# Optimization experiments

Hardware: AMD Instinct MI355X
Metric: run time of the kernel (lower is better)

The kernel has to match this reference:

```python
import jax, jax.numpy as jnp
import numpy as np

D_IN = 1024
D_OUT = 1024
NUM_HEADS = 16
HEAD_DIM = D_OUT // NUM_HEADS


def setup_inputs() -> dict:
    key = jax.random.key(0)
    ks = jax.random.split(key, 6)
    s = 0.02
    x = jax.random.normal(ks[0], (1, 4096, D_IN), dtype=jnp.float32)
    W_q = jax.random.normal(ks[1], (D_IN, D_OUT), dtype=jnp.float32) * s
    W_k = jax.random.normal(ks[2], (D_IN, D_OUT), dtype=jnp.float32) * s
    W_v = jax.random.normal(ks[3], (D_IN, D_OUT), dtype=jnp.float32) * s
    W_o = jax.random.normal(ks[4], (D_OUT, D_OUT), dtype=jnp.float32) * s
    b_o = jnp.zeros((D_OUT,), dtype=jnp.float32)
    return {"x": x, "W_q": W_q, "W_k": W_k, "W_v": W_v, "W_o": W_o, "b_o": b_o}


def reference(x, W_q, W_k, W_v, W_o, b_o):
    b, n, _ = x.shape
    # project and split heads: [b, h, n, d]
    def split_heads(t):
        return t.reshape(b, n, NUM_HEADS, HEAD_DIM).transpose(0, 2, 1, 3)
    q = split_heads(x @ W_q)
    k = split_heads(x @ W_k)
    v = split_heads(x @ W_v)
    scale = 1.0 / jnp.sqrt(jnp.float32(HEAD_DIM))
    scores = jnp.einsum('bhqd,bhkd->bhqk', q, k) * scale  # [b,h,n,n]
    causal = jnp.tril(jnp.ones((n, n), dtype=bool))
    scores = jnp.where(causal, scores, -jnp.inf)
    weights = jax.nn.softmax(scores, axis=-1)
    # dropout rate is 0.0 -> identity
    ctx = jnp.einsum('bhqk,bhkd->bhqd', weights, v)
    ctx = ctx.transpose(0, 2, 1, 3).reshape(b, n, D_OUT)
    return ctx @ W_o + b_o
```

## Files before the change

kernel.cpp:

```cpp
#include <hip/hip_runtime.h>
#include <hip/hip_bf16.h>

typedef __hip_bfloat16 bf16;
typedef __attribute__((ext_vector_type(8))) short short8;
typedef __attribute__((ext_vector_type(4))) short short4v;
typedef __attribute__((ext_vector_type(4))) float floatx4;

#define SEQ 4096
#define DIM 1024
#define NH 16
#define HD 64

__device__ __forceinline__ short f2s(float f) { bf16 t = __float2bfloat16(f); return *(short*)&t; }

__device__ __forceinline__ void gload16(const void* g, void* l) {
    __builtin_amdgcn_global_load_lds(
        (const __attribute__((address_space(1))) void*)g,
        (__attribute__((address_space(3))) void*)l, 16, 0, 0);
}

__device__ __forceinline__ short8 cvt8(float4 a, float4 b) {
    short8 s;
    s[0] = f2s(a.x); s[1] = f2s(a.y); s[2] = f2s(a.z); s[3] = f2s(a.w);
    s[4] = f2s(b.x); s[5] = f2s(b.y); s[6] = f2s(b.z); s[7] = f2s(b.w);
    return s;
}

__global__ __launch_bounds__(256) void transpose_cast_kernel(
    const float* __restrict__ W0, const float* __restrict__ W1,
    const float* __restrict__ W2, const float* __restrict__ W3,
    bf16* __restrict__ Wt_all)
{
    const float* W = blockIdx.z == 0 ? W0 : blockIdx.z == 1 ? W1
                   : blockIdx.z == 2 ? W2 : W3;
    bf16* Wt = Wt_all + (size_t)blockIdx.z * DIM * DIM;

    __shared__ float tile[32][33];
    const int n0 = blockIdx.x * 32, k0 = blockIdx.y * 32;
    const int tr = threadIdx.x >> 5;
    const int tc = threadIdx.x & 31;
#pragma unroll
    for (int i = 0; i < 32; i += 8)
        tile[tr + i][tc] = W[(size_t)(k0 + tr + i) * DIM + n0 + tc];
    __syncthreads();
#pragma unroll
    for (int i = 0; i < 32; i += 8)
        Wt[(size_t)(n0 + tr + i) * DIM + k0 + tc] = __float2bfloat16(tile[tc][tr + i]);
}

#define QBM 128
#define QBN 128
#define QBK 64

__global__ __launch_bounds__(256) void qkv_gemm_kernel(
    const float* __restrict__ A, const bf16* __restrict__ Wt,
    bf16* __restrict__ Qb, bf16* __restrict__ Kb, bf16* __restrict__ Vb)
{
    const int z = blockIdx.z;
    const bf16* Bt = Wt + (size_t)z * DIM * DIM;
    bf16* C = z == 0 ? Qb : (z == 1 ? Kb : Vb);
    const float osc = (z == 0) ? 0.125f : 1.0f;

    __shared__ alignas(16) float Af[QBM][QBK];
    __shared__ alignas(16) short Bs[QBN][QBK];

    const int tid  = threadIdx.x;
    const int wave = tid >> 6, lane = tid & 63;
    const int l15  = lane & 15, quad = lane >> 4;
    const int wm = (wave & 1) * 64;
    const int wn = (wave >> 1) * 64;
    const int bm = blockIdx.y * QBM;
    const int bn = blockIdx.x * QBN;

    const int arow = tid >> 4;
    const int agch = (tid & 15) ^ (arow & 15);
    const float* gA = A + (size_t)(bm + arow) * DIM + agch * 4;
    char* ldsA = (char*)&Af[0][0] + wave * 1024;

    const int brow = tid >> 3;
    const int bgch = (tid & 7) ^ (brow & 7);
    const bf16* gB = Bt + (size_t)(bn + brow) * DIM + bgch * 8;
    char* ldsB = (char*)&Bs[0][0] + wave * 1024;

    floatx4 acc[4][4] = {};

    for (int k0 = 0; k0 < DIM; k0 += QBK) {
        __syncthreads();
#pragma unroll
        for (int c = 0; c < 8; ++c)
            gload16(gA + (size_t)c * 16 * DIM + k0, ldsA + c * 4096);
#pragma unroll
        for (int c = 0; c < 4; ++c)
            gload16(gB + (size_t)c * 32 * DIM + k0, ldsB + c * 4096);
        __syncthreads();

#pragma unroll
        for (int c2 = 0; c2 < 2; ++c2) {
            const int g0 = c2 * 8 + quad * 2;
            const int cb = (c2 * 4 + quad) ^ (l15 & 7);
            short8 afr[4], bfr[4];
#pragma unroll
            for (int i = 0; i < 4; ++i) {
                const int ra = wm + i * 16 + l15;
                float4 f0 = *(const float4*)&Af[ra][(g0 ^ l15) * 4];
                float4 f1 = *(const float4*)&Af[ra][((g0 + 1) ^ l15) * 4];
                afr[i] = cvt8(f0, f1);
                bfr[i] = *(const short8*)&Bs[wn + i * 16 + l15][cb * 8];
            }
#pragma unroll
            for (int mi = 0; mi < 4; ++mi)
#pragma unroll
                for (int ni = 0; ni < 4; ++ni)
                    acc[mi][ni] = __builtin_amdgcn_mfma_f32_16x16x32_bf16(
                        afr[mi], bfr[ni], acc[mi][ni], 0, 0, 0);
        }
    }

#pragma unroll
    for (int mi = 0; mi < 4; ++mi)
#pragma unroll
        for (int r = 0; r < 4; ++r) {
            const int row = bm + wm + mi * 16 + quad * 4 + r;
#pragma unroll
            for (int ni = 0; ni < 4; ++ni) {
                const int col = bn + wn + ni * 16 + l15;
                C[(size_t)row * DIM + col] = __float2bfloat16(acc[mi][ni][r] * osc);
            }
        }
}

__global__ __launch_bounds__(256) void out_gemm_kernel(
    const bf16* __restrict__ A, const bf16* __restrict__ Bt,
    const float* __restrict__ bias, float* __restrict__ C)
{
    __shared__ alignas(16) short Asl[128][64];
    __shared__ alignas(16) short Bsl[64][64];

    const int tid  = threadIdx.x;
    const int wave = tid >> 6, lane = tid & 63;
    const int l15  = lane & 15, quad = lane >> 4;
    const int wm = (wave & 1) * 64;
    const int wn = (wave >> 1) * 32;
    const int bm = blockIdx.y * 128;
    const int bn = blockIdx.x * 64;

    const int srow   = tid >> 3;
    const int gchunk = (tid & 7) ^ (srow & 7);
    const bf16* gA = A  + (size_t)(bm + srow) * DIM + gchunk * 8;
    const bf16* gB = Bt + (size_t)(bn + srow) * DIM + gchunk * 8;
    char* ldsA = (char*)&Asl[0][0] + wave * 1024;
    char* ldsB = (char*)&Bsl[0][0] + wave * 1024;

    floatx4 acc[4][2] = {};

    for (int k0 = 0; k0 < DIM; k0 += 64) {
        __syncthreads();
#pragma unroll
        for (int c = 0; c < 4; ++c)
            gload16(gA + (size_t)c * 32 * DIM + k0, ldsA + c * 4096);
#pragma unroll
        for (int c = 0; c < 2; ++c)
            gload16(gB + (size_t)c * 32 * DIM + k0, ldsB + c * 4096);
        __syncthreads();

#pragma unroll
        for (int c2 = 0; c2 < 2; ++c2) {
            const int cb = (c2 * 4 + quad) ^ (l15 & 7);
            short8 afr[4], bfr[2];
#pragma unroll
            for (int i = 0; i < 4; ++i)
                afr[i] = *(const short8*)&Asl[wm + i * 16 + l15][cb * 8];
#pragma unroll
            for (int i = 0; i < 2; ++i)
                bfr[i] = *(const short8*)&Bsl[wn + i * 16 + l15][cb * 8];
#pragma unroll
            for (int mi = 0; mi < 4; ++mi)
#pragma unroll
                for (int ni = 0; ni < 2; ++ni)
                    acc[mi][ni] = __builtin_amdgcn_mfma_f32_16x16x32_bf16(
                        afr[mi], bfr[ni], acc[mi][ni], 0, 0, 0);
        }
    }

#pragma unroll
    for (int mi = 0; mi < 4; ++mi)
#pragma unroll
        for (int r = 0; r < 4; ++r) {
            const int row = bm + wm + mi * 16 + quad * 4 + r;
#pragma unroll
            for (int ni = 0; ni < 2; ++ni) {
                const int col = bn + wn + ni * 16 + l15;
                C[(size_t)row * DIM + col] = acc[mi][ni][r] + bias[col];
            }
        }
}

#define QT 128
#define KT 64
#define LDT 72

__global__ __launch_bounds__(256) void flash_attn_kernel(
    const bf16* __restrict__ Q, const bf16* __restrict__ K,
    const bf16* __restrict__ V, bf16* ctx)
{
    const int lin  = blockIdx.y * 32 + blockIdx.x;
    const int half = lin >> 8, idx = lin & 255;
    const int qj   = half ? (idx & 31) : 31 - (idx & 31);
    const int h    = (idx >> 5) + 8 * half;
    const int q0   = qj * QT;
    const int nkt  = 2 * qj + 2;

    const int tid  = threadIdx.x;
    const int wave = tid >> 6;
    const int lane = tid & 63;
    const int l15  = lane & 15;
    const int quad = lane >> 4;

    __shared__ alignas(16) short Qs[QT][LDT];
    __shared__ alignas(16) short Ks[2][KT][LDT];
    __shared__ alignas(16) short Vt[2][HD][LDT];
    __shared__ alignas(16) short Ps[4][2][16][LDT];

    {
        const int r = tid >> 1, cb = (tid & 1) * 32;
        const short8* src = (const short8*)(Q + (size_t)(q0 + r) * DIM + h * HD + cb);
#pragma unroll
        for (int i = 0; i < 4; ++i)
            *(short8*)&Qs[r][cb + 8 * i] = src[i];
    }

    const int kr = tid >> 2, kc = (tid & 3) * 16;
    const int vr = (tid & 31) * 2, vd = (tid >> 5) * 8;

    short8 kreg0, kreg1, vreg0, vreg1;
    {
        const short8* kp  = (const short8*)(K + (size_t)kr * DIM + h * HD + kc);
        kreg0 = kp[0]; kreg1 = kp[1];
        const short8* vp0 = (const short8*)(V + (size_t)vr * DIM + h * HD + vd);
        const short8* vp1 = (const short8*)(V + (size_t)(vr + 1) * DIM + h * HD + vd);
        vreg0 = vp0[0]; vreg1 = vp1[0];
    }
    *(short8*)&Ks[0][kr][kc]     = kreg0;
    *(short8*)&Ks[0][kr][kc + 8] = kreg1;
#pragma unroll
    for (int i = 0; i < 8; ++i) {
        unsigned int pv = (unsigned int)(unsigned short)vreg0[i]
                        | ((unsigned int)(unsigned short)vreg1[i] << 16);
        *(unsigned int*)&Vt[0][vd + i][vr] = pv;
    }
    {
        const size_t nb = (size_t)KT;
        const short8* kp  = (const short8*)(K + (nb + kr) * DIM + h * HD + kc);
        kreg0 = kp[0]; kreg1 = kp[1];
        const short8* vp0 = (const short8*)(V + (nb + vr) * DIM + h * HD + vd);
        const short8* vp1 = (const short8*)(V + (nb + vr + 1) * DIM + h * HD + vd);
        vreg0 = vp0[0]; vreg1 = vp1[0];
    }

    __syncthreads();

    short8 qfrag[2][2];
#pragma unroll
    for (int s = 0; s < 2; ++s)
#pragma unroll
        for (int c = 0; c < 2; ++c)
            qfrag[s][c] = *(const short8*)&Qs[wave * 32 + s * 16 + l15][c * 32 + quad * 8];

    short8 onesf;
#pragma unroll
    for (int i = 0; i < 8; ++i) onesf[i] = (short)0x3F80;

    floatx4 o_acc[2][4] = {};
    floatx4 lacc[2] = {};

    for (int kt = 0; kt < nkt; ++kt) {
        const int b = kt & 1;

        floatx4 sT[2][4] = {};
#pragma unroll
        for (int n = 0; n < 4; ++n)
#pragma unroll
            for (int c = 0; c < 2; ++c) {
                short8 kf = *(const short8*)&Ks[b][n * 16 + l15][c * 32 + quad * 8];
#pragma unroll
                for (int s = 0; s < 2; ++s)
                    sT[s][n] = __builtin_amdgcn_mfma_f32_16x16x32_bf16(
                        kf, qfrag[s][c], sT[s][n], 0, 0, 0);
            }

        const int kbase = kt * KT;
        if (kt >= nkt - 2) {
#pragma unroll
            for (int s = 0; s < 2; ++s) {
                const int qrow = q0 + wave * 32 + s * 16 + l15;
#pragma unroll
                for (int n = 0; n < 4; ++n) {
                    const int key0 = kbase + n * 16 + quad * 4;
                    short4v pk;
#pragma unroll
                    for (int r = 0; r < 4; ++r) {
                        float p = (key0 + r <= qrow) ? __expf(sT[s][n][r]) : 0.f;
                        pk[r] = f2s(p);
                    }
                    *(short4v*)&Ps[wave][s][l15][n * 16 + quad * 4] = pk;
                }
            }
        } else {
#pragma unroll
            for (int s = 0; s < 2; ++s)
#pragma unroll
                for (int n = 0; n < 4; ++n) {
                    short4v pk;
#pragma unroll
                    for (int r = 0; r < 4; ++r)
                        pk[r] = f2s(__expf(sT[s][n][r]));
                    *(short4v*)&Ps[wave][s][l15][n * 16 + quad * 4] = pk;
                }
        }

        short8 pfrag[2][2];
#pragma unroll
        for (int s = 0; s < 2; ++s) {
            pfrag[s][0] = *(const short8*)&Ps[wave][s][l15][quad * 8];
            pfrag[s][1] = *(const short8*)&Ps[wave][s][l15][32 + quad * 8];
        }
#pragma unroll
        for (int n = 0; n < 4; ++n)
#pragma unroll
            for (int c = 0; c < 2; ++c) {
                short8 vf = *(const short8*)&Vt[b][n * 16 + l15][c * 32 + quad * 8];
#pragma unroll
                for (int s = 0; s < 2; ++s)
                    o_acc[s][n] = __builtin_amdgcn_mfma_f32_16x16x32_bf16(
                        pfrag[s][c], vf, o_acc[s][n], 0, 0, 0);
            }
#pragma unroll
        for (int s = 0; s < 2; ++s) {
            lacc[s] = __builtin_amdgcn_mfma_f32_16x16x32_bf16(pfrag[s][0], onesf, lacc[s], 0, 0, 0);
            lacc[s] = __builtin_amdgcn_mfma_f32_16x16x32_bf16(pfrag[s][1], onesf, lacc[s], 0, 0, 0);
        }

        if (kt + 1 < nkt) {
            *(short8*)&Ks[b ^ 1][kr][kc]     = kreg0;
            *(short8*)&Ks[b ^ 1][kr][kc + 8] = kreg1;
#pragma unroll
            for (int i = 0; i < 8; ++i) {
                unsigned int pv = (unsigned int)(unsigned short)vreg0[i]
                                | ((unsigned int)(unsigned short)vreg1[i] << 16);
                *(unsigned int*)&Vt[b ^ 1][vd + i][vr] = pv;
            }
            if (kt + 2 < nkt) {
                const size_t nb = (size_t)(kt + 2) * KT;
                const short8* kp  = (const short8*)(K + (nb + kr) * DIM + h * HD + kc);
                kreg0 = kp[0]; kreg1 = kp[1];
                const short8* vp0 = (const short8*)(V + (nb + vr) * DIM + h * HD + vd);
                const short8* vp1 = (const short8*)(V + (nb + vr + 1) * DIM + h * HD + vd);
                vreg0 = vp0[0]; vreg1 = vp1[0];
            }
        }
        __syncthreads();
    }

#pragma unroll
    for (int s = 0; s < 2; ++s)
#pragma unroll
        for (int r = 0; r < 4; ++r) {
            const float inv = 1.0f / lacc[s][r];
            const int row = q0 + wave * 32 + s * 16 + quad * 4 + r;
#pragma unroll
            for (int n = 0; n < 4; ++n)
                ctx[(size_t)row * DIM + h * HD + n * 16 + l15] =
                    __float2bfloat16(o_acc[s][n][r] * inv);
        }
}

extern "C" void kernel_launch(void* const* d_in, const int* in_sizes, int n_in,
                              void* d_out, int out_size, void* d_ws, size_t ws_size,
                              hipStream_t stream)
{
    const float* x  = (const float*)d_in[0];
    const float* Wq = (const float*)d_in[1];
    const float* Wk = (const float*)d_in[2];
    const float* Wv = (const float*)d_in[3];
    const float* Wo = (const float*)d_in[4];
    const float* bo = (const float*)d_in[5];
    float* out = (float*)d_out;

    bf16* Wt_all = (bf16*)d_ws;
    bf16* Qb     = Wt_all + (size_t)4 * DIM * DIM;
    bf16* V      = (bf16*)d_out;
    bf16* Kb     = V + (size_t)SEQ * DIM;
    bf16* ctx    = Qb;
    const bf16* Wot = Wt_all + (size_t)3 * DIM * DIM;

    transpose_cast_kernel<<<dim3(32, 32, 4), 256, 0, stream>>>(Wq, Wk, Wv, Wo, Wt_all);

    qkv_gemm_kernel<<<dim3(DIM / QBN, SEQ / QBM, 3), 256, 0, stream>>>(
        x, Wt_all, Qb, Kb, V);

    flash_attn_kernel<<<dim3(32, NH), 256, 0, stream>>>(Qb, Kb, V, ctx);

    out_gemm_kernel<<<dim3(DIM / 64, SEQ / 128), 256, 0, stream>>>(
        ctx, Wot, bo, out);
}
```

Measured before the change: 198.3 us.

## Pre-cast x to bf16 for async LDS QKV GEMM; swizzle attention LDS tiles

Adds a separate kernel that casts x to bf16 once. A new QKV GEMM then streams bf16 A and B tiles straight into LDS with global_load_lds, using an XOR swizzle, so each of the three projection blocks no longer converts fp32 x itself. The flash attention kernel replaces its padded LDS arrays with XOR-swizzled unpadded tiles and reuses the Q buffer to stage P, which cuts shared-memory footprint and bank conflicts. The new path runs only when the workspace is large enough, and it costs an extra launch plus extra memory traffic for the bf16 copy of x.

```diff
diff --git a/kernel.cpp b/kernel.cpp
--- a/kernel.cpp
+++ b/kernel.cpp
@@ -24,6 +24,14 @@
     s[0] = f2s(a.x); s[1] = f2s(a.y); s[2] = f2s(a.z); s[3] = f2s(a.w);
     s[4] = f2s(b.x); s[5] = f2s(b.y); s[6] = f2s(b.z); s[7] = f2s(b.w);
     return s;
+}
+
+__global__ __launch_bounds__(256) void cast_x_kernel(
+    const float* __restrict__ x, bf16* __restrict__ xb)
+{
+    const int i = (blockIdx.x * 256 + threadIdx.x) * 8;
+    const float4* p = (const float4*)(x + i);
+    *(short8*)(xb + i) = cvt8(p[0], p[1]);
 }
 
 __global__ __launch_bounds__(256) void transpose_cast_kernel(
@@ -129,6 +137,79 @@
         }
 }
 
+__global__ __launch_bounds__(256) void qkv_gemm_bf16_kernel(
+    const bf16* __restrict__ A, const bf16* __restrict__ Wt,
+    bf16* __restrict__ Qb, bf16* __restrict__ Kb, bf16* __restrict__ Vb)
+{
+    const int z = blockIdx.z;
+    const bf16* Bt = Wt + (size_t)z * DIM * DIM;
+    bf16* C = z == 0 ? Qb : (z == 1 ? Kb : Vb);
+    const float osc = (z == 0) ? 0.125f : 1.0f;
+
+    __shared__ alignas(16) short Asl[QBM][QBK];
+    __shared__ alignas(16) short Bsl[QBN][QBK];
+
+    const int tid  = threadIdx.x;
+    const int wave = tid >> 6, lane = tid & 63;
+    const int l15  = lane & 15, quad = lane >> 4;
+    const int wm = (wave & 1) * 64;
+    const int wn = (wave >> 1) * 64;
+    const int bm = blockIdx.y * QBM;
+    const int bn = blockIdx.x * QBN;
+
+    const int srow   = tid >> 3;
+    const int gchunk = (tid & 7) ^ (srow & 7);
+    const bf16* gA = A  + (size_t)(bm + srow) * DIM + gchunk * 8;
+    const bf16* gB = Bt + (size_t)(bn + srow) * DIM + gchunk * 8;
+    char* ldsA = (char*)&Asl[0][0] + wave * 1024;
+    char* ldsB = (char*)&Bsl[0][0] + wave * 1024;
+
+    const int ca0 = ((quad)     ^ (l15 & 7)) * 8;
+    const int ca1 = ((quad + 4) ^ (l15 & 7)) * 8;
+
+    floatx4 acc[4][4] = {};
+
+    for (int k0 = 0; k0 < DIM; k0 += QBK) {
+        __syncthreads();
+#pragma unroll
+        for (int c = 0; c < 4; ++c) {
+            gload16(gA + (size_t)c * 32 * DIM + k0, ldsA + c * 4096);
+            gload16(gB + (size_t)c * 32 * DIM + k0, ldsB + c * 4096);
+        }
+        __syncthreads();
+
+        short8 afr[4][2], bfr[4][2];
+#pragma unroll
+        for (int i = 0; i < 4; ++i) {
+            afr[i][0] = *(const short8*)&Asl[wm + i * 16 + l15][ca0];
+            afr[i][1] = *(const short8*)&Asl[wm + i * 16 + l15][ca1];
+            bfr[i][0] = *(const short8*)&Bsl[wn + i * 16 + l15][ca0];
+            bfr[i][1] = *(const short8*)&Bsl[wn + i * 16 + l15][ca1];
+        }
+#pragma unroll
+        for (int mi = 0; mi < 4; ++mi)
+#pragma unroll
+            for (int ni = 0; ni < 4; ++ni) {
+                acc[mi][ni] = __builtin_amdgcn_mfma_f32_16x16x32_bf16(
+                    afr[mi][0], bfr[ni][0], acc[mi][ni], 0, 0, 0);
+                acc[mi][ni] = __builtin_amdgcn_mfma_f32_16x16x32_bf16(
+                    afr[mi][1], bfr[ni][1], acc[mi][ni], 0, 0, 0);
+            }
+    }
+
+#pragma unroll
+    for (int mi = 0; mi < 4; ++mi)
+#pragma unroll
+        for (int r = 0; r < 4; ++r) {
+            const int row = bm + wm + mi * 16 + quad * 4 + r;
+#pragma unroll
+            for (int ni = 0; ni < 4; ++ni) {
+                const int col = bn + wn + ni * 16 + l15;
+                C[(size_t)row * DIM + col] = __float2bfloat16(acc[mi][ni][r] * osc);
+            }
+        }
+}
+
 __global__ __launch_bounds__(256) void out_gemm_kernel(
     const bf16* __restrict__ A, const bf16* __restrict__ Bt,
     const float* __restrict__ bias, float* __restrict__ C)
@@ -197,7 +278,6 @@
 
 #define QT 128
 #define KT 64
-#define LDT 72
 
 __global__ __launch_bounds__(256) void flash_attn_kernel(
     const bf16* __restrict__ Q, const bf16* __restrict__ K,
@@ -215,42 +295,45 @@
     const int lane = tid & 63;
     const int l15  = lane & 15;
     const int quad = lane >> 4;
-
-    __shared__ alignas(16) short Qs[QT][LDT];
-    __shared__ alignas(16) short Ks[2][KT][LDT];
-    __shared__ alignas(16) short Vt[2][HD][LDT];
-    __shared__ alignas(16) short Ps[4][2][16][LDT];
+    const int le   = l15 & 7;
+
+    __shared__ alignas(16) short QP[128 * 64];
+    __shared__ alignas(16) short Ks[2][64 * 64];
+    __shared__ alignas(16) short Vt[2][64 * 64];
 
     {
-        const int r = tid >> 1, cb = (tid & 1) * 32;
-        const short8* src = (const short8*)(Q + (size_t)(q0 + r) * DIM + h * HD + cb);
-#pragma unroll
-        for (int i = 0; i < 4; ++i)
-            *(short8*)&Qs[r][cb + 8 * i] = src[i];
-    }
-
-    const int kr = tid >> 2, kc = (tid & 3) * 16;
-    const int vr = (tid & 31) * 2, vd = (tid >> 5) * 8;
+        const int r = tid >> 1, e = r & 7;
+        const short8* src = (const short8*)(Q + (size_t)(q0 + r) * DIM + h * HD + (tid & 1) * 32);
+#pragma unroll
+        for (int i = 0; i < 4; ++i) {
+            const int c = (tid & 1) * 4 + i;
+            *(short8*)&QP[r * 64 + ((c ^ e) * 8)] = src[i];
+        }
+    }
+
+    const int kr = tid >> 2, ke = kr & 7, kc0 = (tid & 3) * 2;
+    const int vw = tid & 31, vd = (tid >> 5) * 8, vr = vw * 2;
 
     short8 kreg0, kreg1, vreg0, vreg1;
     {
-        const short8* kp  = (const short8*)(K + (size_t)kr * DIM + h * HD + kc);
+        const short8* kp  = (const short8*)(K + (size_t)kr * DIM + h * HD + kc0 * 8);
         kreg0 = kp[0]; kreg1 = kp[1];
         const short8* vp0 = (const short8*)(V + (size_t)vr * DIM + h * HD + vd);
         const short8* vp1 = (const short8*)(V + (size_t)(vr + 1) * DIM + h * HD + vd);
         vreg0 = vp0[0]; vreg1 = vp1[0];
     }
-    *(short8*)&Ks[0][kr][kc]     = kreg0;
-    *(short8*)&Ks[0][kr][kc + 8] = kreg1;
+    *(short8*)&Ks[0][kr * 64 + ((kc0 ^ ke) * 8)]       = kreg0;
+    *(short8*)&Ks[0][kr * 64 + (((kc0 + 1) ^ ke) * 8)] = kreg1;
 #pragma unroll
     for (int i = 0; i < 8; ++i) {
         unsigned int pv = (unsigned int)(unsigned short)vreg0[i]
                         | ((unsigned int)(unsigned short)vreg1[i] << 16);
-        *(unsigned int*)&Vt[0][vd + i][vr] = pv;
+        const int row = vd + i;
+        *(unsigned int*)&Vt[0][row * 64 + (((vw >> 2) ^ (row & 7)) * 8) + (vw & 3) * 2] = pv;
     }
     {
         const size_t nb = (size_t)KT;
-        const short8* kp  = (const short8*)(K + (nb + kr) * DIM + h * HD + kc);
+        const short8* kp  = (const short8*)(K + (nb + kr) * DIM + h * HD + kc0 * 8);
         kreg0 = kp[0]; kreg1 = kp[1];
         const short8* vp0 = (const short8*)(V + (nb + vr) * DIM + h * HD + vd);
         const short8* vp1 = (const short8*)(V + (nb + vr + 1) * DIM + h * HD + vd);
@@ -264,7 +347,8 @@
     for (int s = 0; s < 2; ++s)
 #pragma unroll
         for (int c = 0; c < 2; ++c)
-            qfrag[s][c] = *(const short8*)&Qs[wave * 32 + s * 16 + l15][c * 32 + quad * 8];
+            qfrag[s][c] = *(const short8*)&QP[(wave * 32 + s * 16 + l15) * 64
+                                              + (((c * 4 + quad) ^ le) * 8)];
 
     short8 onesf;
 #pragma unroll
@@ -272,6 +356,7 @@
 
     floatx4 o_acc[2][4] = {};
     floatx4 lacc[2] = {};
+    const int prow = wave * 32 + l15;
 
     for (int kt = 0; kt < nkt; ++kt) {
         const int b = kt & 1;
@@ -281,7 +366,8 @@
         for (int n = 0; n < 4; ++n)
 #pragma unroll
             for (int c = 0; c < 2; ++c) {
-                short8 kf = *(const short8*)&Ks[b][n * 16 + l15][c * 32 + quad * 8];
+                short8 kf = *(const short8*)&Ks[b][(n * 16 + l15) * 64
+                                                   + (((c * 4 + quad) ^ le) * 8)];
 #pragma unroll
                 for (int s = 0; s < 2; ++s)
                     sT[s][n] = __builtin_amdgcn_mfma_f32_16x16x32_bf16(
@@ -298,11 +384,10 @@
                     const int key0 = kbase + n * 16 + quad * 4;
                     short4v pk;
 #pragma unroll
-                    for (int r = 0; r < 4; ++r) {
-                        float p = (key0 + r <= qrow) ? __expf(sT[s][n][r]) : 0.f;
-                        pk[r] = f2s(p);
-                    }
-                    *(short4v*)&Ps[wave][s][l15][n * 16 + quad * 4] = pk;
+                    for (int r = 0; r < 4; ++r)
+                        pk[r] = f2s((key0 + r <= qrow) ? __expf(sT[s][n][r]) : 0.f);
+                    *(short4v*)&QP[(prow + s * 16) * 64
+                                   + (((n * 2 + (quad >> 1)) ^ le) * 8) + (quad & 1) * 4] = pk;
                 }
             }
         } else {
@@ -314,21 +399,24 @@
 #pragma unroll
                     for (int r = 0; r < 4; ++r)
                         pk[r] = f2s(__expf(sT[s][n][r]));
-                    *(short4v*)&Ps[wave][s][l15][n * 16 + quad * 4] = pk;
+                    *(short4v*)&QP[(prow + s * 16) * 64
+                                   + (((n * 2 + (quad >> 1)) ^ le) * 8) + (quad & 1) * 4] = pk;
                 }
         }
 
         short8 pfrag[2][2];
 #pragma unroll
-        for (int s = 0; s < 2; ++s) {
-            pfrag[s][0] = *(const short8*)&Ps[wave][s][l15][quad * 8];
-            pfrag[s][1] = *(const short8*)&Ps[wave][s][l15][32 + quad * 8];
-        }
+        for (int s = 0; s < 2; ++s)
+#pragma unroll
+            for (int c = 0; c < 2; ++c)
+                pfrag[s][c] = *(const short8*)&QP[(prow + s * 16) * 64
+                                                  + (((c * 4 + quad) ^ le) * 8)];
 #pragma unroll
         for (int n = 0; n < 4; ++n)
 #pragma unroll
             for (int c = 0; c < 2; ++c) {
-                short8 vf = *(const short8*)&Vt[b][n * 16 + l15][c * 32 + quad * 8];
+                short8 vf = *(const short8*)&Vt[b][(n * 16 + l15) * 64
+                                                   + (((c * 4 + quad) ^ le) * 8)];
 #pragma unroll
                 for (int s = 0; s < 2; ++s)
                     o_acc[s][n] = __builtin_amdgcn_mfma_f32_16x16x32_bf16(
@@ -341,17 +429,18 @@
         }
 
         if (kt + 1 < nkt) {
-            *(short8*)&Ks[b ^ 1][kr][kc]     = kreg0;
-            *(short8*)&Ks[b ^ 1][kr][kc + 8] = kreg1;
+            *(short8*)&Ks[b ^ 1][kr * 64 + ((kc0 ^ ke) * 8)]       = kreg0;
+            *(short8*)&Ks[b ^ 1][kr * 64 + (((kc0 + 1) ^ ke) * 8)] = kreg1;
 #pragma unroll
             for (int i = 0; i < 8; ++i) {
                 unsigned int pv = (unsigned int)(unsigned short)vreg0[i]
                                 | ((unsigned int)(unsigned short)vreg1[i] << 16);
-                *(unsigned int*)&Vt[b ^ 1][vd + i][vr] = pv;
+                const int row = vd + i;
+                *(unsigned int*)&Vt[b ^ 1][row * 64 + (((vw >> 2) ^ (row & 7)) * 8) + (vw & 3) * 2] = pv;
             }
             if (kt + 2 < nkt) {
                 const size_t nb = (size_t)(kt + 2) * KT;
-                const short8* kp  = (const short8*)(K + (nb + kr) * DIM + h * HD + kc);
+                const short8* kp  = (const short8*)(K + (nb + kr) * DIM + h * HD + kc0 * 8);
                 kreg0 = kp[0]; kreg1 = kp[1];
                 const short8* vp0 = (const short8*)(V + (nb + vr) * DIM + h * HD + vd);
                 const short8* vp1 = (const short8*)(V + (nb + vr + 1) * DIM + h * HD + vd);
@@ -395,8 +484,15 @@
 
     transpose_cast_kernel<<<dim3(32, 32, 4), 256, 0, stream>>>(Wq, Wk, Wv, Wo, Wt_all);
 
-    qkv_gemm_kernel<<<dim3(DIM / QBN, SEQ / QBM, 3), 256, 0, stream>>>(
-        x, Wt_all, Qb, Kb, V);
+    if (ws_size >= (size_t)24 * 1024 * 1024) {
+        bf16* xb = Qb + (size_t)SEQ * DIM;
+        cast_x_kernel<<<dim3(SEQ * DIM / 2048), 256, 0, stream>>>(x, xb);
+        qkv_gemm_bf16_kernel<<<dim3(DIM / QBN, SEQ / QBM, 3), 256, 0, stream>>>(
+            xb, Wt_all, Qb, Kb, V);
+    } else {
+        qkv_gemm_kernel<<<dim3(DIM / QBN, SEQ / QBM, 3), 256, 0, stream>>>(
+            x, Wt_all, Qb, Kb, V);
+    }
 
     flash_attn_kernel<<<dim3(32, NH), 256, 0, stream>>>(Qb, Kb, V, ctx);
 
```

After: 204.2 us. +3.0%, slower.
